# Optimization experiments

Hardware: AMD Instinct MI355X
Metric: run time of the kernel (lower is better)

## Reference

```python
import jax, jax.numpy as jnp
import numpy as np

B, T, D, H = 2, 1024, 1024, 16
K = D            # key_dim = hidden * expand_k (1.0)
V = 2 * D        # value_dim = hidden * expand_v (2.0)
DK, DV = K // H, V // H
I = 2816         # SwiGLU intermediate
CONV = 4
EPS = 1e-6


def rmsnorm(x, w, eps=EPS):
    return x * jax.lax.rsqrt(jnp.mean(x * x, -1, keepdims=True) + eps) * w


def l2norm(x, eps=EPS):
    return x * jax.lax.rsqrt(jnp.sum(x * x, -1, keepdims=True) + eps)


def short_conv(x, w):
    # depthwise causal conv1d (kernel CONV, no bias) + silu; x [B,T,C], w [C,CONV]
    kern = w.T[:, None, :]  # [CONV, 1, C]
    y = jax.lax.conv_general_dilated(
        x, kern, (1,), [(CONV - 1, 0)],
        dimension_numbers=('NWC', 'WIO', 'NWC'),
        feature_group_count=x.shape[-1])
    return jax.nn.silu(y)


def setup_inputs() -> dict:
    key = jax.random.key(0)
    ks = jax.random.split(key, 20)
    p = lambda i, shape, s=0.02: jax.random.normal(ks[i], shape, jnp.float32) * s
    return dict(
        x=jax.random.normal(ks[0], (B, T, D), jnp.float32),
        norm1_w=jnp.ones((D,), jnp.float32),
        wq=p(1, (D, K)), wk=p(2, (D, K)), wv=p(3, (D, V)),
        conv_q=p(4, (K, CONV), 0.3), conv_k=p(5, (K, CONV), 0.3), conv_v=p(6, (V, CONV), 0.3),
        wb=p(7, (D, H)), wa=p(8, (D, H)),
        A_log=jnp.log(jax.random.uniform(ks[9], (H,), jnp.float32, 1.0, 16.0)),
        dt_bias=jnp.log(jnp.expm1(jax.random.uniform(ks[10], (H,), jnp.float32, 0.001, 0.1))),
        wg=p(11, (D, V)),
        o_norm_w=jnp.ones((DV,), jnp.float32),
        wo=p(12, (V, D)),
        norm2_w=jnp.ones((D,), jnp.float32),
        w1=p(13, (D, I)), w2=p(14, (I, D)), w3=p(15, (D, I)),
    )


def reference(x, norm1_w, wq, wk, wv, conv_q, conv_k, conv_v, wb, wa,
              A_log, dt_bias, wg, o_norm_w, wo, norm2_w, w1, w2, w3):
    h = rmsnorm(x, norm1_w)
    # projections + short causal conv (silu)
    q = short_conv(h @ wq, conv_q).reshape(B, T, H, DK)
    k = short_conv(h @ wk, conv_k).reshape(B, T, H, DK)
    v = short_conv(h @ wv, conv_v).reshape(B, T, H, DV)
    q = l2norm(q) * (DK ** -0.5)
    k = l2norm(k)
    beta = jax.nn.sigmoid(h @ wb)                              # [B,T,H]
    # mamba-style decay gate: g = -exp(A_log) * softplus(a + dt_bias)
    g = -jnp.exp(A_log) * jax.nn.softplus(h @ wa + dt_bias)   # [B,T,H]

    # gated delta rule: S_t = exp(g_t)*S_{t-1}; u_t = beta_t*(v_t - k_t^T S_t);
    # S_t += k_t u_t^T; o_t = q_t^T S_t
    def step(S, inp):
        qt, kt, vt, gt, bt = inp                               # [B,H,*]
        S = S * jnp.exp(gt)[..., None, None]
        u = (vt - jnp.einsum('bhk,bhkv->bhv', kt, S)) * bt[..., None]
        S = S + kt[..., None] * u[:, :, None, :]
        ot = jnp.einsum('bhk,bhkv->bhv', qt, S)
        return S, ot

    S0 = jnp.zeros((B, H, DK, DV), x.dtype)
    seq = (q.transpose(1, 0, 2, 3), k.transpose(1, 0, 2, 3),
           v.transpose(1, 0, 2, 3), g.transpose(1, 0, 2), beta.transpose(1, 0, 2))
    _, o = jax.lax.scan(step, S0, seq)
    o = o.transpose(1, 0, 2, 3)                                # [B,T,H,DV]

    # output gate: per-head RMSNorm * swish(gate), then out-projection
    gate = (h @ wg).reshape(B, T, H, DV)
    o = rmsnorm(o, o_norm_w) * gate * jax.nn.sigmoid(gate)
    x = x + o.reshape(B, T, V) @ wo

    # SwiGLU MLP with residual
    h2 = rmsnorm(x, norm2_w)
    return x + (jax.nn.silu(h2 @ w1) * (h2 @ w3)) @ w2
```

## Files before the change

kernel.cpp:

```cpp
#include <hip/hip_runtime.h>
#include <stdint.h>

typedef unsigned short u16;
typedef float f32x4 __attribute__((ext_vector_type(4)));
typedef __bf16 bf16x8 __attribute__((ext_vector_type(8)));
typedef unsigned short u16x8 __attribute__((ext_vector_type(8)));

#define N1P 6400

__device__ __forceinline__ u16 f2bf(float f) {
    union { float f; uint32_t u; } v; v.f = f;
    uint32_t u = v.u;
    return (u16)((u + 0x7FFFu + ((u >> 16) & 1u)) >> 16);
}
__device__ __forceinline__ float bf2f(u16 h) {
    union { uint32_t u; float f; } v; v.u = ((uint32_t)h) << 16; return v.f;
}
__device__ __forceinline__ float sigm(float x) { return 1.f / (1.f + __expf(-x)); }

__device__ __forceinline__ void async16(const u16* g, u16* l) {
    __builtin_amdgcn_global_load_lds((const __attribute__((address_space(1))) void*)g,
                                     (__attribute__((address_space(3))) void*)l, 16, 0, 0);
}

__device__ __forceinline__ int swz64(int row, int col) {
    return row * 128 + ((((col >> 3) ^ (row & 7)) << 3) + (col & 7)) * 2;
}
__device__ __forceinline__ bf16x8 frag64(const u16* m, int rowbase, int lane, int kk) {
    const int row = rowbase + (lane & 15);
    const int unit = (lane >> 4) + (kk << 2);
    return *(const bf16x8*)((const char*)m + row * 128 + ((unit ^ (row & 7)) << 4));
}

struct TJob { const float* src; u16* dst; int rows, cols, rowOff, rowStride, nOut, blkBase, gx, mode; };
struct TJobs { TJob j[10]; };

__global__ __launch_bounds__(256) void k_transpose_all(TJobs jobs, int njobs) {
    __shared__ float tile[32][33];
    const int bid = blockIdx.x;
    int ji = 0;
#pragma unroll
    for (int i = 1; i < 10; ++i)
        if (i < njobs && bid >= jobs.j[i].blkBase) ji = i;
    const TJob J = jobs.j[ji];
    const int bx = bid - J.blkBase;
    const int n0 = (bx % J.gx) * 32, k0 = (bx / J.gx) * 32;
    const int tx = threadIdx.x, ty = threadIdx.y;
#pragma unroll
    for (int j = 0; j < 32; j += 8) {
        int r = k0 + ty + j, c = n0 + tx;
        tile[ty + j][tx] = (r < J.rows && c < J.cols) ? J.src[(size_t)r * J.cols + c] : 0.f;
    }
    __syncthreads();
#pragma unroll
    for (int j = 0; j < 32; j += 8) {
        int n = n0 + ty + j, k = k0 + tx;
        if (n < J.nOut) {
            int drow = (J.mode == 0) ? (J.rowOff + n * J.rowStride)
                                     : (J.rowOff + ((n >> 4) << 5) + (n & 15));
            J.dst[(size_t)drow * J.rows + k] = f2bf(tile[tx][ty + j]);
        }
    }
}

__global__ __launch_bounds__(256) void k_rmsnorm(const float* __restrict__ x, const float* __restrict__ w,
                                                 u16* __restrict__ out) {
    const int row = blockIdx.x, tid = threadIdx.x, lane = tid & 63, wave = tid >> 6;
    const float4 v = ((const float4*)(x + (size_t)row * 1024))[tid];
    float ss = v.x * v.x + v.y * v.y + v.z * v.z + v.w * v.w;
#pragma unroll
    for (int o = 1; o < 64; o <<= 1) ss += __shfl_xor(ss, o);
    __shared__ float sred[4];
    if (lane == 0) sred[wave] = ss;
    __syncthreads();
    const float tot = sred[0] + sred[1] + sred[2] + sred[3];
    const float rn = rsqrtf(tot * (1.f / 1024.f) + 1e-6f);
    const float4 wv = ((const float4*)w)[tid];
    uint2 pk;
    pk.x = (uint32_t)f2bf(v.x * rn * wv.x) | ((uint32_t)f2bf(v.y * rn * wv.y) << 16);
    pk.y = (uint32_t)f2bf(v.z * rn * wv.z) | ((uint32_t)f2bf(v.w * rn * wv.w) << 16);
    *(uint2*)&out[(size_t)row * 1024 + tid * 4] = pk;
}

template <int EPI>
__global__ __launch_bounds__(512, 2) void k_gemm256(const u16* __restrict__ A, const u16* __restrict__ Bt,
                                                    u16* __restrict__ Cout, int N, int Kd) {
    __shared__ __align__(16) u16 L[65536];
    const int q8 = (int)gridDim.x >> 3;
    const int bid = blockIdx.x;
    const int wg = (bid & 7) * q8 + (bid >> 3);
    const int bm = wg & 7, bn = wg >> 3;
    const int tid = threadIdx.x, lane = tid & 63, wave = tid >> 6;
    const int wm = wave >> 2, wn = wave & 3;

    const int scol = ((tid & 7) ^ ((tid >> 3) & 7)) * 8;
    const u16* gA = A + (size_t)(bm * 256 + (tid >> 3)) * Kd + scol;
    const u16* gB = Bt + (size_t)(bn * 256 + (tid >> 3)) * Kd + scol;
    u16* dstT = L + tid * 8;

    const int NT = Kd >> 6;
    const int NI = NT >> 1;

    auto issue = [&](const u16* g, int mtx, int kt, int h) {
        u16* d = dstT + (kt & 1) * 32768 + mtx * 16384 + h * 8192;
        const u16* s = g + (size_t)(h * 128) * Kd + kt * 64;
        async16(s, d);
        async16(s + (size_t)64 * Kd, d + 4096);
    };

    issue(gB, 1, 0, 0); issue(gB, 1, 0, 1);
    issue(gA, 0, 0, 0); issue(gA, 0, 0, 1);
    issue(gB, 1, 1, 0); issue(gB, 1, 1, 1);
    asm volatile("s_waitcnt vmcnt(4)" ::: "memory");
    __builtin_amdgcn_s_barrier();

    f32x4 acc[8][4] = {};
    bf16x8 bq[4][2];

    for (int i = 0; i < NI; ++i) {
        const int kt0 = 2 * i;
#pragma unroll
        for (int p = 0; p < 8; ++p) {
            const int half = p >> 2;
            const int q = p & 3;
            const u16* Ab = L + half * 32768;
            const u16* Bb = L + half * 32768 + 16384;
            if (q == 0) {
#pragma unroll
                for (int ni = 0; ni < 4; ++ni)
#pragma unroll
                    for (int kk = 0; kk < 2; ++kk)
                        bq[ni][kk] = frag64(Bb, wn * 64 + ni * 16, lane, kk);
            }
            bf16x8 af[2][2];
#pragma unroll
            for (int j = 0; j < 2; ++j)
#pragma unroll
                for (int kk = 0; kk < 2; ++kk)
                    af[j][kk] = frag64(Ab, wm * 128 + (2 * q + j) * 16, lane, kk);
            if (p == 0) { if (kt0 + 1 < NT) issue(gA, 0, kt0 + 1, 0); }
            if (p == 1) { if (kt0 + 1 < NT) issue(gA, 0, kt0 + 1, 1);
                          if (kt0 + 2 < NT) issue(gB, 1, kt0 + 2, 0); }
            if (p == 2) { if (kt0 + 2 < NT) issue(gB, 1, kt0 + 2, 1); }
            if (p == 4) { if (kt0 + 2 < NT) issue(gA, 0, kt0 + 2, 0); }
            if (p == 5) { if (kt0 + 2 < NT) issue(gA, 0, kt0 + 2, 1);
                          if (kt0 + 3 < NT) issue(gB, 1, kt0 + 3, 0); }
            if (p == 6) { if (kt0 + 3 < NT) issue(gB, 1, kt0 + 3, 1); }
            if (p == 3) { if (i + 1 < NI) { asm volatile("s_waitcnt vmcnt(4)" ::: "memory"); }
                          else            { asm volatile("s_waitcnt vmcnt(0)" ::: "memory"); } }
            if (p == 7) { if (i + 1 < NI) { asm volatile("s_waitcnt vmcnt(4)" ::: "memory"); } }
            __builtin_amdgcn_s_barrier();
            __builtin_amdgcn_s_setprio(1);
#pragma unroll
            for (int j = 0; j < 2; ++j)
#pragma unroll
                for (int ni = 0; ni < 4; ++ni)
#pragma unroll
                    for (int kk = 0; kk < 2; ++kk)
                        acc[2 * q + j][ni] = __builtin_amdgcn_mfma_f32_16x16x32_bf16(
                            af[j][kk], bq[ni][kk], acc[2 * q + j][ni], 0, 0, 0);
            __builtin_amdgcn_s_setprio(0);
            __builtin_amdgcn_s_barrier();
        }
    }

    const int rsub = (lane >> 4) * 4, csub = lane & 15;
    if constexpr (EPI == 2) {
        u16* ct = L;
#pragma unroll
        for (int r = 0; r < 2; ++r) {
            if (wm == r) {
#pragma unroll
                for (int mi = 0; mi < 8; ++mi)
#pragma unroll
                    for (int ni = 0; ni < 4; ++ni)
#pragma unroll
                        for (int rr = 0; rr < 4; ++rr)
                            ct[(mi * 16 + rsub + rr) * 264 + wn * 64 + ni * 16 + csub] =
                                f2bf(acc[mi][ni][rr]);
            }
            __syncthreads();
#pragma unroll
            for (int k = 0; k < 8; ++k) {
                const int f = (tid + k * 512) * 8;
                const int r2 = f >> 8, c = f & 255;
                *(u16x8*)&Cout[(size_t)(bm * 256 + r * 128 + r2) * N + bn * 256 + c] =
                    *(const u16x8*)&ct[r2 * 264 + c];
            }
            __syncthreads();
        }
    } else {
        u16* ct = L;
#pragma unroll
        for (int mi = 0; mi < 8; ++mi)
#pragma unroll
            for (int g = 0; g < 2; ++g)
#pragma unroll
                for (int rr = 0; rr < 4; ++rr) {
                    const float u1 = acc[mi][2 * g][rr];
                    const float u3 = acc[mi][2 * g + 1][rr];
                    ct[(wm * 128 + mi * 16 + rsub + rr) * 132 + wn * 32 + g * 16 + csub] =
                        f2bf(u1 * sigm(u1) * u3);
                }
        __syncthreads();
#pragma unroll
        for (int k = 0; k < 8; ++k) {
            const int f = (tid + k * 512) * 8;
            const int r2 = f >> 7, c = f & 127;
            *(u16x8*)&Cout[(size_t)(bm * 256 + r2) * N + bn * 128 + c] =
                *(const u16x8*)&ct[r2 * 132 + c];
        }
    }
}

__global__ __launch_bounds__(512) void k_gemm_skinny(const u16* __restrict__ A, const u16* __restrict__ Bt,
                                                     float* __restrict__ Cout, const float* __restrict__ Res,
                                                     int N, int Kd) {
    __shared__ __align__(16) char smem[49152];
    u16* Asb = (u16*)smem;
    u16* Bsb = (u16*)(smem + 32768);
    const int q = (int)gridDim.x >> 3;
    const int bid = blockIdx.x;
    const int wg = (bid & 7) * q + (bid >> 3);
    const int bm = wg & 15, bn = wg >> 4;
    const int tid = threadIdx.x, lane = tid & 63, wave = tid >> 6;
    const int wm = wave >> 1, wn = wave & 1;

    const int srow = tid >> 3;
    const int scol = ((tid & 7) ^ ((tid >> 3) & 7)) * 8;
    const u16* gA = A + (size_t)(bm * 128 + srow) * Kd + scol;
    const u16* gB = Bt + (size_t)(bn * 64 + srow) * Kd + scol;

    f32x4 acc[2][2] = {};
    const int NT = Kd >> 6;

    async16(gA, Asb + wave * 512);
    async16(gA + (size_t)64 * Kd, Asb + 4096 + wave * 512);
    async16(gB, Bsb + wave * 512);
    asm volatile("s_waitcnt vmcnt(0)" ::: "memory");
    __syncthreads();

    int buf = 0;
    for (int t = 0; t < NT; ++t) {
        if (t + 1 < NT) {
            const int k0 = (t + 1) << 6;
            const int ba = (buf ^ 1) * 8192, bb2 = (buf ^ 1) * 4096;
            async16(gA + k0, Asb + ba + wave * 512);
            async16(gA + (size_t)64 * Kd + k0, Asb + ba + 4096 + wave * 512);
            async16(gB + k0, Bsb + bb2 + wave * 512);
        }
        const u16* Ab = Asb + buf * 8192;
        const u16* Bb = Bsb + buf * 4096;
#pragma unroll
        for (int kk = 0; kk < 2; ++kk) {
            bf16x8 af[2], bfr[2];
#pragma unroll
            for (int mi = 0; mi < 2; ++mi) af[mi] = frag64(Ab, wm * 32 + mi * 16, lane, kk);
#pragma unroll
            for (int ni = 0; ni < 2; ++ni) bfr[ni] = frag64(Bb, wn * 32 + ni * 16, lane, kk);
#pragma unroll
            for (int mi = 0; mi < 2; ++mi)
#pragma unroll
                for (int ni = 0; ni < 2; ++ni)
                    acc[mi][ni] = __builtin_amdgcn_mfma_f32_16x16x32_bf16(af[mi], bfr[ni], acc[mi][ni], 0, 0, 0);
        }
        asm volatile("s_waitcnt vmcnt(0)" ::: "memory");
        __syncthreads();
        buf ^= 1;
    }

    const int rsub = (lane >> 4) * 4;
    const int csub = lane & 15;
    float* ctile = (float*)smem;
#pragma unroll
    for (int mi = 0; mi < 2; ++mi)
#pragma unroll
        for (int ni = 0; ni < 2; ++ni)
#pragma unroll
            for (int r = 0; r < 4; ++r)
                ctile[(wm * 32 + mi * 16 + rsub + r) * 68 + wn * 32 + ni * 16 + csub] = acc[mi][ni][r];
    __syncthreads();
#pragma unroll
    for (int k = 0; k < 4; ++k) {
        const int f = (tid + k * 512) * 4;
        const int r = f >> 6, c = f & 63;
        float4 v = *(const float4*)&ctile[r * 68 + c];
        const float4 rv = *(const float4*)&Res[(size_t)(bm * 128 + r) * N + bn * 64 + c];
        v.x += rv.x; v.y += rv.y; v.z += rv.z; v.w += rv.w;
        *(float4*)&Cout[(size_t)(bm * 128 + r) * N + bn * 64 + c] = v;
    }
}

__global__ __launch_bounds__(256) void k_conv(const u16* __restrict__ P, const float* __restrict__ cwq,
                                              const float* __restrict__ cwk, const float* __restrict__ cwv,
                                              const float* __restrict__ A_log, const float* __restrict__ dtb,
                                              u16* __restrict__ Qb, u16* __restrict__ Kb,
                                              u16* __restrict__ Vb, float* __restrict__ Gl,
                                              float* __restrict__ Bbuf) {
    const int bid = blockIdx.x;
    const int row = (bid & 7) * 256 + (bid >> 3);
    const int t = row & 1023;
    const int tid = threadIdx.x;
    const long prow = (long)row * N1P;
#pragma unroll
    for (int p = 0; p < 2; ++p) {
        const int g = p * 256 + tid;
        const int c = g * 8;
        u16x8 taps[4];
#pragma unroll
        for (int j = 0; j < 4; ++j) {
            const int tt = t - 3 + j;
            if (tt >= 0) taps[j] = *(const u16x8*)&P[prow + (long)(j - 3) * N1P + c];
            else         taps[j] = u16x8{};
        }
        const float* cw = (c < 1024) ? (cwq + c * 4)
                          : (c < 2048) ? (cwk + (c - 1024) * 4)
                                       : (cwv + (c - 2048) * 4);
        float y[8];
#pragma unroll
        for (int e = 0; e < 8; ++e) {
            const float4 w = ((const float4*)cw)[e];
            float v = bf2f(taps[0][e]) * w.x + bf2f(taps[1][e]) * w.y +
                      bf2f(taps[2][e]) * w.z + bf2f(taps[3][e]) * w.w;
            y[e] = v * sigm(v);
        }
        if (c < 2048) {
            float ss = 0.f;
#pragma unroll
            for (int e = 0; e < 8; ++e) ss += y[e] * y[e];
            ss += __shfl_xor(ss, 1); ss += __shfl_xor(ss, 2); ss += __shfl_xor(ss, 4);
            const float rn = rsqrtf(ss + 1e-6f);
            const float sc = (c < 1024) ? rn * 0.125f : rn;
            u16x8 o;
#pragma unroll
            for (int e = 0; e < 8; ++e) o[e] = f2bf(y[e] * sc);
            if (c < 1024) *(u16x8*)&Qb[(size_t)row * 1024 + c] = o;
            else          *(u16x8*)&Kb[(size_t)row * 1024 + (c - 1024)] = o;
        } else {
            u16x8 o;
#pragma unroll
            for (int e = 0; e < 8; ++e) o[e] = f2bf(y[e]);
            *(u16x8*)&Vb[(size_t)row * 2048 + (c - 2048)] = o;
        }
    }
    if (tid < 32) {
        const int h = tid & 15;
        const float val = bf2f(P[prow + 4096 + tid]);
        if (tid < 16) {
            Bbuf[(size_t)row * 16 + h] = sigm(val);
        } else {
            const float a = val + dtb[h];
            const float sp = (a > 15.f) ? a : log1pf(__expf(a));
            Gl[(size_t)row * 16 + h] = -__expf(A_log[h]) * sp;
        }
    }
}

__global__ __launch_bounds__(256) void k_scan1(
    const u16* __restrict__ Qb, const u16* __restrict__ Kb, const u16* __restrict__ Vb,
    const float* __restrict__ Gl, const float* __restrict__ Bb,
    u16* __restrict__ CHW, u16* __restrict__ CHM, u16* __restrict__ CHQc,
    u16* __restrict__ CHKcT, u16* __restrict__ CHU0T, float* __restrict__ CHcC) {
    __shared__ __align__(16) char sm[66048];
    u16* Ql   = (u16*)(sm);
    u16* Kl   = (u16*)(sm + 8192);
    u16* VTb  = (u16*)(sm + 16384);
    u16* KT1b = (u16*)(sm + 32768);
    u16* Mim  = (u16*)(sm + 40960);
    u16* MTim = (u16*)(sm + 49152);
    u16* Tb   = (u16*)(sm + 57344);
    float* Tl    = (float*)sm;
    float* gcs   = (float*)(sm + 65536);
    float* betal = (float*)(sm + 65792);

    const int blk = blockIdx.x;
    const int bb = blk >> 8, h = (blk >> 4) & 15, ch = blk & 15;
    const int bhc = blk;
    const int tid = threadIdx.x, lane = tid & 63, wave = tid >> 6;
    const long rowbase = (long)bb * 1024 + ch * 64;

    if (tid < 64) {
        gcs[tid] = Gl[(rowbase + tid) * 16 + h];
        betal[tid] = Bb[(rowbase + tid) * 16 + h];
    }
    for (int u = tid; u < 512; u += 256) {
        int r = u >> 3, c8 = u & 7;
        uint4 kv = *(const uint4*)&Kb[(rowbase + r) * 1024 + h * 64 + c8 * 8];
        uint4 qv = *(const uint4*)&Qb[(rowbase + r) * 1024 + h * 64 + c8 * 8];
        int b = r * 128 + ((c8 ^ (r & 7)) << 4);
        *(uint4*)((char*)Kl + b) = kv;
        *(uint4*)((char*)Ql + b) = qv;
    }
    __syncthreads();
    if (wave == 0) {
        float g = gcs[lane];
#pragma unroll
        for (int off = 1; off < 64; off <<= 1) {
            float n = __shfl_up(g, off, 64);
            if (lane >= off) g += n;
        }
        gcs[lane] = g;
    }
    for (int u = tid; u < 1024; u += 256) {
        int r = u >> 4, c8 = u & 15;
        u16x8 vv = *(const u16x8*)&Vb[(rowbase + r) * 2048 + h * 128 + c8 * 8];
        float bsc = betal[r];
#pragma unroll
        for (int j = 0; j < 8; ++j) {
            int dv = c8 * 8 + j;
            *(u16*)((char*)VTb + swz64(dv, r)) = f2bf(bf2f(vv[j]) * bsc);
        }
    }
    f32x4 aQK[4] = {}, aKK[4] = {};
#pragma unroll
    for (int nt = 0; nt < 4; ++nt)
#pragma unroll
        for (int kk = 0; kk < 2; ++kk) {
            bf16x8 bq = frag64(Kl, nt * 16, lane, kk);
            aQK[nt] = __builtin_amdgcn_mfma_f32_16x16x32_bf16(frag64(Ql, wave * 16, lane, kk), bq, aQK[nt], 0, 0, 0);
            aKK[nt] = __builtin_amdgcn_mfma_f32_16x16x32_bf16(frag64(Kl, wave * 16, lane, kk), bq, aKK[nt], 0, 0, 0);
        }
    __syncthreads();

    const float gcsC = gcs[63];
    float am[4][4];
#pragma unroll
    for (int nt = 0; nt < 4; ++nt)
#pragma unroll
        for (int reg = 0; reg < 4; ++reg) {
            int t = wave * 16 + ((lane >> 4) << 2) + reg;
            int i = nt * 16 + (lane & 15);
            float dec = __expf(gcs[t] - gcs[i]);
            float mv = (i <= t) ? dec * aQK[nt][reg] : 0.f;
            *(u16*)((char*)CHM + (size_t)bhc * 8192 + swz64(t, i)) = f2bf(mv);
            float a = (i < t) ? betal[t] * dec * aKK[nt][reg] : 0.f;
            am[nt][reg] = -a;
            u16 amb = f2bf(-a);
            *(u16*)((char*)Mim + swz64(t, i)) = amb;
            *(u16*)((char*)MTim + swz64(i, t)) = amb;
        }
    for (int e = tid; e < 4096; e += 256) {
        int r = e >> 6, c = e & 63;
        int ib = swz64(r, c);
        float qv = bf2f(*(const u16*)((const char*)Ql + ib)) * __expf(gcs[r]);
        *(u16*)((char*)CHQc + (size_t)bhc * 8192 + ib) = f2bf(qv);
        float kv = bf2f(*(const u16*)((const char*)Kl + ib));
        int ob = swz64(c, r);
        *(u16*)((char*)KT1b + ob) = f2bf(kv * betal[r] * __expf(gcs[r]));
        *(u16*)((char*)CHKcT + (size_t)bhc * 8192 + ob) = f2bf(kv * __expf(gcsC - gcs[r]));
    }
    if (tid == 0) CHcC[bhc] = __expf(gcsC);
    __syncthreads();

#pragma unroll
    for (int nt = 0; nt < 4; ++nt)
#pragma unroll
        for (int reg = 0; reg < 4; ++reg) {
            int t = wave * 16 + ((lane >> 4) << 2) + reg;
            int i = nt * 16 + (lane & 15);
            float tv = (t == i) ? 1.f : am[nt][reg];
            Tl[t * 64 + i] = tv;
            *(u16*)((char*)Tb + swz64(t, i)) = f2bf(tv);
        }
    __syncthreads();

    const int hi = wave * 16 + 15;
#pragma unroll
    for (int j = 1; j <= 5; ++j) {
        f32x4 aM[4] = {};
#pragma unroll
        for (int nt = 0; nt < 4; ++nt) {
            if (nt * 16 > hi - (1 << j)) continue;
#pragma unroll
            for (int kk = 0; kk < 2; ++kk) {
                if (kk * 32 > hi) break;
                aM[nt] = __builtin_amdgcn_mfma_f32_16x16x32_bf16(
                    frag64(Mim, wave * 16, lane, kk), frag64(MTim, nt * 16, lane, kk), aM[nt], 0, 0, 0);
            }
        }
        __syncthreads();
#pragma unroll
        for (int nt = 0; nt < 4; ++nt)
#pragma unroll
            for (int reg = 0; reg < 4; ++reg) {
                int t = wave * 16 + ((lane >> 4) << 2) + reg;
                int i = nt * 16 + (lane & 15);
                float mv = (t - i >= (1 << j)) ? aM[nt][reg] : 0.f;
                u16 mb = f2bf(mv);
                *(u16*)((char*)Mim + swz64(t, i)) = mb;
                *(u16*)((char*)MTim + swz64(i, t)) = mb;
            }
        __syncthreads();
        f32x4 aT[4];
#pragma unroll
        for (int nt = 0; nt < 4; ++nt)
#pragma unroll
            for (int reg = 0; reg < 4; ++reg) {
                int t = wave * 16 + ((lane >> 4) << 2) + reg;
                int i = nt * 16 + (lane & 15);
                aT[nt][reg] = Tl[t * 64 + i];
            }
#pragma unroll
        for (int nt = 0; nt < 4; ++nt) {
            if (nt * 16 > hi - (1 << j)) continue;
#pragma unroll
            for (int kk = 0; kk < 2; ++kk) {
                if (kk * 32 > hi) break;
                aT[nt] = __builtin_amdgcn_mfma_f32_16x16x32_bf16(
                    frag64(Tb, wave * 16, lane, kk), frag64(MTim, nt * 16, lane, kk), aT[nt], 0, 0, 0);
            }
        }
#pragma unroll
        for (int nt = 0; nt < 4; ++nt)
#pragma unroll
            for (int reg = 0; reg < 4; ++reg) {
                int t = wave * 16 + ((lane >> 4) << 2) + reg;
                int i = nt * 16 + (lane & 15);
                Tl[t * 64 + i] = aT[nt][reg];
                *(u16*)((char*)Tb + swz64(t, i)) = f2bf(aT[nt][reg]);
            }
    }
    __syncthreads();

    {
        f32x4 aW[4] = {};
#pragma unroll
        for (int nt = 0; nt < 4; ++nt)
#pragma unroll
            for (int kk = 0; kk < 2; ++kk) {
                if (kk * 32 > hi) break;
                aW[nt] = __builtin_amdgcn_mfma_f32_16x16x32_bf16(
                    frag64(Tb, wave * 16, lane, kk), frag64(KT1b, nt * 16, lane, kk), aW[nt], 0, 0, 0);
            }
#pragma unroll
        for (int nt = 0; nt < 4; ++nt)
#pragma unroll
            for (int reg = 0; reg < 4; ++reg) {
                int r = wave * 16 + ((lane >> 4) << 2) + reg;
                int c = nt * 16 + (lane & 15);
                *(u16*)((char*)CHW + (size_t)bhc * 8192 + swz64(r, c)) = f2bf(aW[nt][reg]);
            }
    }
#pragma unroll
    for (int rt = 0; rt < 2; ++rt) {
        f32x4 aU[4] = {};
        int rb = (wave * 2 + rt) * 16;
#pragma unroll
        for (int nt = 0; nt < 4; ++nt)
#pragma unroll
            for (int kk = 0; kk < 2; ++kk) {
                if (kk * 32 > nt * 16 + 15) continue;
                aU[nt] = __builtin_amdgcn_mfma_f32_16x16x32_bf16(
                    frag64(VTb, rb, lane, kk), frag64(Tb, nt * 16, lane, kk), aU[nt], 0, 0, 0);
            }
#pragma unroll
        for (int nt = 0; nt < 4; ++nt)
#pragma unroll
            for (int reg = 0; reg < 4; ++reg) {
                int dv = rb + ((lane >> 4) << 2) + reg;
                int c = nt * 16 + (lane & 15);
                *(u16*)((char*)CHU0T + (size_t)bhc * 16384 + swz64(dv, c)) = f2bf(aU[nt][reg]);
            }
    }
}

__global__ __launch_bounds__(256) void k_scan2(
    const u16* __restrict__ CHW, const u16* __restrict__ CHKcT, const u16* __restrict__ CHU0T,
    const float* __restrict__ CHcC, u16* __restrict__ CHu, u16* __restrict__ CHS0) {
    __shared__ __align__(16) u16 stg[2][3 * 4096];
    __shared__ __align__(16) u16 STb[4096], uTl[4096];
    __shared__ float ST[64 * 66];
    const int blk = blockIdx.x;
    const int bb = blk >> 5, h = (blk >> 1) & 15, dvh = blk & 1;
    const int bh = bb * 16 + h;
    const int tid = threadIdx.x, lane = tid & 63, wave = tid >> 6;

    for (int e = tid; e < 64 * 66; e += 256) ST[e] = 0.f;
    for (int e = tid; e < 4096; e += 256) STb[e] = 0;

    auto stage = [&](int buf, int ch) {
        const size_t base = (size_t)(bh * 16 + ch);
        const u16* srcs[3] = { CHW + base * 4096, CHKcT + base * 4096,
                               CHU0T + base * 8192 + dvh * 4096 };
#pragma unroll
        for (int s = 0; s < 3; ++s)
#pragma unroll
            for (int r = 0; r < 2; ++r) {
                int ub = r * 256 + wave * 64;
                async16(srcs[s] + (size_t)(ub + lane) * 8, &stg[buf][s * 4096 + ub * 8]);
            }
    };
    stage(0, 0);
    for (int ch = 0; ch < 16; ++ch) {
        const int cur = ch & 1;
        asm volatile("s_waitcnt vmcnt(0)" ::: "memory");
        __syncthreads();
        if (ch < 15) stage(cur ^ 1, ch + 1);
        const u16* sW = &stg[cur][0];
        const u16* sKcT = &stg[cur][4096];
        const u16* sU0 = &stg[cur][8192];
        {
            f32x4 acc[4] = {};
#pragma unroll
            for (int nt = 0; nt < 4; ++nt)
#pragma unroll
                for (int kk = 0; kk < 2; ++kk)
                    acc[nt] = __builtin_amdgcn_mfma_f32_16x16x32_bf16(
                        frag64(STb, wave * 16, lane, kk), frag64(sW, nt * 16, lane, kk), acc[nt], 0, 0, 0);
            const size_t ubase = ((size_t)(bh * 16 + ch) * 2 + dvh) * 8192;
#pragma unroll
            for (int nt = 0; nt < 4; ++nt)
#pragma unroll
                for (int reg = 0; reg < 4; ++reg) {
                    int dv = wave * 16 + ((lane >> 4) << 2) + reg;
                    int c = nt * 16 + (lane & 15);
                    int b = swz64(dv, c);
                    float u0 = bf2f(*(const u16*)((const char*)sU0 + b));
                    u16 uv = f2bf(u0 - acc[nt][reg]);
                    *(u16*)((char*)uTl + b) = uv;
                    *(u16*)((char*)CHu + ubase + b) = uv;
                }
        }
        __syncthreads();
        f32x4 accS[4] = {};
#pragma unroll
        for (int nt = 0; nt < 4; ++nt)
#pragma unroll
            for (int kk = 0; kk < 2; ++kk)
                accS[nt] = __builtin_amdgcn_mfma_f32_16x16x32_bf16(
                    frag64(uTl, wave * 16, lane, kk), frag64(sKcT, nt * 16, lane, kk), accS[nt], 0, 0, 0);
        __syncthreads();
        const float cC = CHcC[bh * 16 + ch];
        const size_t sbase = ((size_t)(bh * 16 + ch + 1) * 2 + dvh) * 8192;
#pragma unroll
        for (int nt = 0; nt < 4; ++nt)
#pragma unroll
            for (int reg = 0; reg < 4; ++reg) {
                int rr = wave * 16 + ((lane >> 4) << 2) + reg;
                int cc = nt * 16 + (lane & 15);
                float ns = cC * ST[rr * 66 + cc] + accS[nt][reg];
                ST[rr * 66 + cc] = ns;
                u16 nb = f2bf(ns);
                *(u16*)((char*)STb + swz64(rr, cc)) = nb;
                if (ch < 15) *(u16*)((char*)CHS0 + sbase + swz64(rr, cc)) = nb;
            }
    }
}

__global__ __launch_bounds__(256) void k_scan3(
    const u16* __restrict__ CHM, const u16* __restrict__ CHQc, const u16* __restrict__ CHu,
    const u16* __restrict__ CHS0, const u16* __restrict__ P, const float* __restrict__ onw,
    u16* __restrict__ OG) {
    __shared__ __align__(16) char sm3[65536];
    u16* sM  = (u16*)sm3;
    u16* sQc = (u16*)(sm3 + 8192);
    u16* sU  = (u16*)(sm3 + 16384);
    u16* sS0 = (u16*)(sm3 + 32768);
    u16* sPg = (u16*)(sm3 + 49152);
    const int blk = blockIdx.x;
    const int bb = blk >> 8, h = (blk >> 4) & 15, ch = blk & 15;
    const size_t bhc = blk;
    const int tid = threadIdx.x, lane = tid & 63, wave = tid >> 6;
    const bool hasS0 = (ch != 0);

#pragma unroll
    for (int r = 0; r < 2; ++r) {
        const int ub = r * 256 + wave * 64;
        async16(CHM + bhc * 4096 + (size_t)(ub + lane) * 8, sM + ub * 8);
        async16(CHQc + bhc * 4096 + (size_t)(ub + lane) * 8, sQc + ub * 8);
#pragma unroll
        for (int d = 0; d < 2; ++d) {
            async16(CHu + (bhc * 2 + d) * 4096 + (size_t)(ub + lane) * 8, sU + d * 4096 + ub * 8);
            if (hasS0)
                async16(CHS0 + (bhc * 2 + d) * 4096 + (size_t)(ub + lane) * 8, sS0 + d * 4096 + ub * 8);
        }
    }
    const long prow0 = ((long)bb * 1024 + ch * 64) * N1P + 4128 + h * 128;
#pragma unroll
    for (int k = 0; k < 4; ++k) {
        const int i = tid + k * 256;
        const int row = i >> 4, seg = i & 15;
        async16(P + prow0 + (long)row * N1P + seg * 8, sPg + i * 8);
    }
    asm volatile("s_waitcnt vmcnt(0)" ::: "memory");
    __syncthreads();

    f32x4 accO[2][4] = {};
#pragma unroll
    for (int d = 0; d < 2; ++d)
#pragma unroll
        for (int nt = 0; nt < 4; ++nt)
#pragma unroll
            for (int kk = 0; kk < 2; ++kk) {
                accO[d][nt] = __builtin_amdgcn_mfma_f32_16x16x32_bf16(
                    frag64(sM, wave * 16, lane, kk), frag64(sU + d * 4096, nt * 16, lane, kk),
                    accO[d][nt], 0, 0, 0);
                if (hasS0)
                    accO[d][nt] = __builtin_amdgcn_mfma_f32_16x16x32_bf16(
                        frag64(sQc, wave * 16, lane, kk), frag64(sS0 + d * 4096, nt * 16, lane, kk),
                        accO[d][nt], 0, 0, 0);
            }

    const int rsub = (lane >> 4) * 4, csub = lane & 15;
    float rn[4];
#pragma unroll
    for (int reg = 0; reg < 4; ++reg) {
        float ss = 0.f;
#pragma unroll
        for (int d = 0; d < 2; ++d)
#pragma unroll
            for (int nt = 0; nt < 4; ++nt) {
                const float v = accO[d][nt][reg];
                ss += v * v;
            }
        ss += __shfl_xor(ss, 1); ss += __shfl_xor(ss, 2);
        ss += __shfl_xor(ss, 4); ss += __shfl_xor(ss, 8);
        rn[reg] = rsqrtf(ss * (1.f / 128.f) + 1e-6f);
    }
    __syncthreads();
    u16* ct = (u16*)sm3;
#pragma unroll
    for (int d = 0; d < 2; ++d)
#pragma unroll
        for (int nt = 0; nt < 4; ++nt)
#pragma unroll
            for (int reg = 0; reg < 4; ++reg) {
                const int rr = wave * 16 + rsub + reg;
                const int dv = d * 64 + nt * 16 + csub;
                const float g = bf2f(sPg[rr * 128 + dv]);
                const float val = accO[d][nt][reg] * rn[reg] * onw[dv] * g * sigm(g);
                ct[rr * 136 + dv] = f2bf(val);
            }
    __syncthreads();
#pragma unroll
    for (int k = 0; k < 4; ++k) {
        const int f = (tid + k * 256) * 8;
        const int r2 = f >> 7, c = f & 127;
        *(u16x8*)&OG[(size_t)(bb * 1024 + ch * 64 + r2) * 2048 + h * 128 + c] =
            *(const u16x8*)&ct[r2 * 136 + c];
    }
}

extern "C" void kernel_launch(void* const* d_in, const int* in_sizes, int n_in,
                              void* d_out, int out_size, void* d_ws, size_t ws_size,
                              hipStream_t stream) {
    const float* x   = (const float*)d_in[0];
    const float* n1w = (const float*)d_in[1];
    const float* wq  = (const float*)d_in[2];
    const float* wk  = (const float*)d_in[3];
    const float* wv  = (const float*)d_in[4];
    const float* cq  = (const float*)d_in[5];
    const float* ck  = (const float*)d_in[6];
    const float* cv  = (const float*)d_in[7];
    const float* wb  = (const float*)d_in[8];
    const float* wa  = (const float*)d_in[9];
    const float* Alg = (const float*)d_in[10];
    const float* dtb = (const float*)d_in[11];
    const float* wg  = (const float*)d_in[12];
    const float* onw = (const float*)d_in[13];
    const float* wo  = (const float*)d_in[14];
    const float* n2w = (const float*)d_in[15];
    const float* w1  = (const float*)d_in[16];
    const float* w2  = (const float*)d_in[17];
    const float* w3  = (const float*)d_in[18];

    if (ws_size < 128190464ULL) return;

    char* ws = (char*)d_ws;
    u16*   WcatT = (u16*)(ws + 0);
    u16*   WoT   = (u16*)(ws + 13107200);
    u16*   W13T  = (u16*)(ws + 17301504);
    u16*   W2T   = (u16*)(ws + 28835840);
    u16*   hA    = (u16*)(ws + 34603008);
    u16*   P     = (u16*)(ws + 38797312);
    u16*   Qb    = (u16*)(ws + 65011712);
    u16*   Kb    = (u16*)(ws + 69206016);
    u16*   Vb    = (u16*)(ws + 73400320);
    float* Gl    = (float*)(ws + 81788928);
    float* Bbf   = (float*)(ws + 81920000);
    float* X2    = (float*)(ws + 82051072);
    u16*   CHKcT = (u16*)(ws + 98828288);
    u16*   CHU0T = (u16*)(ws + 103022592);
    float* CHcC  = (float*)(ws + 111411200);
    u16*   CHu   = (u16*)(ws + 111413248);
    u16*   CHS0  = (u16*)(ws + 119801856);
    u16*   CHW   = WcatT;
    u16*   CHM   = (u16*)(ws + 4194304);
    u16*   CHQc  = (u16*)(ws + 8388608);
    u16*   Mm  = Qb;
    u16*   OG  = Vb;
    u16*   h2A = hA;

    TJobs tj;
    tj.j[0] = { wq, WcatT, 1024, 1024,    0, 1, 1024,     0, 32, 0 };
    tj.j[1] = { wk, WcatT, 1024, 1024, 1024, 1, 1024,  1024, 32, 0 };
    tj.j[2] = { wv, WcatT, 1024, 2048, 2048, 1, 2048,  2048, 64, 0 };
    tj.j[3] = { wb, WcatT, 1024,   16, 4096, 1,   16,  4096,  1, 0 };
    tj.j[4] = { wa, WcatT, 1024,   16, 4112, 1,   16,  4128,  1, 0 };
    tj.j[5] = { wg, WcatT, 1024, 2048, 4128, 1, 2272,  4160, 71, 0 };
    tj.j[6] = { wo, WoT,   2048, 1024,    0, 1, 1024,  6432, 32, 0 };
    tj.j[7] = { w1, W13T,  1024, 2816,    0, 1, 2816,  8480, 88, 1 };
    tj.j[8] = { w3, W13T,  1024, 2816,   16, 1, 2816, 11296, 88, 1 };
    tj.j[9] = { w2, W2T,   2816, 1024,    0, 1, 1024, 14112, 32, 0 };
    k_transpose_all<<<16928, dim3(32, 8), 0, stream>>>(tj, 10);

    k_rmsnorm<<<2048, 256, 0, stream>>>(x, n1w, hA);
    k_gemm256<2><<<200, 512, 0, stream>>>(hA, WcatT, P, N1P, 1024);

    k_conv<<<2048, 256, 0, stream>>>(P, cq, ck, cv, Alg, dtb, Qb, Kb, Vb, Gl, Bbf);

    k_scan1<<<512, 256, 0, stream>>>(Qb, Kb, Vb, Gl, Bbf, CHW, CHM, CHQc, CHKcT, CHU0T, CHcC);
    k_scan2<<<64, 256, 0, stream>>>(CHW, CHKcT, CHU0T, CHcC, CHu, CHS0);
    k_scan3<<<512, 256, 0, stream>>>(CHM, CHQc, CHu, CHS0, P, onw, OG);

    k_gemm_skinny<<<256, 512, 0, stream>>>(OG, WoT, X2, x, 1024, 2048);

    k_rmsnorm<<<2048, 256, 0, stream>>>(X2, n2w, h2A);
    k_gemm256<3><<<176, 512, 0, stream>>>(h2A, W13T, Mm, 2816, 1024);
    k_gemm_skinny<<<256, 512, 0, stream>>>(Mm, W2T, (float*)d_out, X2, 1024, 2816);
}
```

Measured before the change: 259.0 us.

## Precompute chunk transition matrices in scan1 to shorten sequential scan2 chain

Rewrites the inter-chunk state recurrence algebraically. scan1 now precomputes per chunk A = -W^T KcT and B = U0^T KcT, so scan2 performs a single matmul per chunk (S·A + B, plus the decayed old state) instead of two dependent matmuls with an intermediate u write. The u correction (U0 - S0·W) moves into the parallel scan3 kernel. This takes work off the serial 64-block scan2 in exchange for extra MFMA work and global writes in scan1 and scan3, and it adds one more bf16 rounding of the transition matrix A.

```diff
diff --git a/kernel.cpp b/kernel.cpp
--- a/kernel.cpp
+++ b/kernel.cpp
@@ -360,7 +360,8 @@
     const u16* __restrict__ Qb, const u16* __restrict__ Kb, const u16* __restrict__ Vb,
     const float* __restrict__ Gl, const float* __restrict__ Bb,
     u16* __restrict__ CHW, u16* __restrict__ CHM, u16* __restrict__ CHQc,
-    u16* __restrict__ CHKcT, u16* __restrict__ CHU0T, float* __restrict__ CHcC) {
+    u16* __restrict__ CHKcT, u16* __restrict__ CHU0T, float* __restrict__ CHcC,
+    u16* __restrict__ CHA2m, u16* __restrict__ CHB) {
     __shared__ __align__(16) char sm[66048];
     u16* Ql   = (u16*)(sm);
     u16* Kl   = (u16*)(sm + 8192);
@@ -522,6 +523,15 @@
     }
     __syncthreads();
 
+    u16* KcTl = Ql;
+    u16* WTl  = Kl;
+    u16* U0Tl = Mim;
+#pragma unroll
+    for (int r = 0; r < 2; ++r) {
+        const int g = r * 256 + tid;
+        async16(CHKcT + (size_t)bhc * 4096 + (size_t)g * 8, KcTl + g * 8);
+    }
+
     {
         f32x4 aW[4] = {};
 #pragma unroll
@@ -538,7 +548,9 @@
             for (int reg = 0; reg < 4; ++reg) {
                 int r = wave * 16 + ((lane >> 4) << 2) + reg;
                 int c = nt * 16 + (lane & 15);
-                *(u16*)((char*)CHW + (size_t)bhc * 8192 + swz64(r, c)) = f2bf(aW[nt][reg]);
+                u16 wv = f2bf(aW[nt][reg]);
+                *(u16*)((char*)CHW + (size_t)bhc * 8192 + swz64(r, c)) = wv;
+                *(u16*)((char*)WTl + swz64(c, r)) = wv;
             }
     }
 #pragma unroll
@@ -559,16 +571,57 @@
             for (int reg = 0; reg < 4; ++reg) {
                 int dv = rb + ((lane >> 4) << 2) + reg;
                 int c = nt * 16 + (lane & 15);
-                *(u16*)((char*)CHU0T + (size_t)bhc * 16384 + swz64(dv, c)) = f2bf(aU[nt][reg]);
+                u16 uv = f2bf(aU[nt][reg]);
+                *(u16*)((char*)CHU0T + (size_t)bhc * 16384 + swz64(dv, c)) = uv;
+                *(u16*)((char*)U0Tl + swz64(dv, c)) = uv;
+            }
+    }
+    asm volatile("s_waitcnt vmcnt(0)" ::: "memory");
+    __syncthreads();
+
+    {
+        f32x4 aA[4] = {};
+#pragma unroll
+        for (int nt = 0; nt < 4; ++nt)
+#pragma unroll
+            for (int kk = 0; kk < 2; ++kk)
+                aA[nt] = __builtin_amdgcn_mfma_f32_16x16x32_bf16(
+                    frag64(WTl, wave * 16, lane, kk), frag64(KcTl, nt * 16, lane, kk), aA[nt], 0, 0, 0);
+#pragma unroll
+        for (int nt = 0; nt < 4; ++nt)
+#pragma unroll
+            for (int reg = 0; reg < 4; ++reg) {
+                int kI = wave * 16 + ((lane >> 4) << 2) + reg;
+                int dk = nt * 16 + (lane & 15);
+                *(u16*)((char*)CHA2m + (size_t)bhc * 8192 + swz64(dk, kI)) = f2bf(-aA[nt][reg]);
+            }
+    }
+#pragma unroll
+    for (int rt = 0; rt < 2; ++rt) {
+        f32x4 aB[4] = {};
+        int rb = (wave * 2 + rt) * 16;
+#pragma unroll
+        for (int nt = 0; nt < 4; ++nt)
+#pragma unroll
+            for (int kk = 0; kk < 2; ++kk)
+                aB[nt] = __builtin_amdgcn_mfma_f32_16x16x32_bf16(
+                    frag64(U0Tl, rb, lane, kk), frag64(KcTl, nt * 16, lane, kk), aB[nt], 0, 0, 0);
+#pragma unroll
+        for (int nt = 0; nt < 4; ++nt)
+#pragma unroll
+            for (int reg = 0; reg < 4; ++reg) {
+                int dv = rb + ((lane >> 4) << 2) + reg;
+                int dk = nt * 16 + (lane & 15);
+                *(u16*)((char*)CHB + (size_t)bhc * 16384 + swz64(dv, dk)) = f2bf(aB[nt][reg]);
             }
     }
 }
 
 __global__ __launch_bounds__(256) void k_scan2(
-    const u16* __restrict__ CHW, const u16* __restrict__ CHKcT, const u16* __restrict__ CHU0T,
-    const float* __restrict__ CHcC, u16* __restrict__ CHu, u16* __restrict__ CHS0) {
-    __shared__ __align__(16) u16 stg[2][3 * 4096];
-    __shared__ __align__(16) u16 STb[4096], uTl[4096];
+    const u16* __restrict__ CHA2m, const u16* __restrict__ CHB,
+    const float* __restrict__ CHcC, u16* __restrict__ CHS0) {
+    __shared__ __align__(16) u16 stg[2][8192];
+    __shared__ __align__(16) u16 STb[4096];
     __shared__ float ST[64 * 66];
     const int blk = blockIdx.x;
     const int bb = blk >> 5, h = (blk >> 1) & 15, dvh = blk & 1;
@@ -580,83 +633,60 @@
 
     auto stage = [&](int buf, int ch) {
         const size_t base = (size_t)(bh * 16 + ch);
-        const u16* srcs[3] = { CHW + base * 4096, CHKcT + base * 4096,
-                               CHU0T + base * 8192 + dvh * 4096 };
-#pragma unroll
-        for (int s = 0; s < 3; ++s)
-#pragma unroll
-            for (int r = 0; r < 2; ++r) {
-                int ub = r * 256 + wave * 64;
-                async16(srcs[s] + (size_t)(ub + lane) * 8, &stg[buf][s * 4096 + ub * 8]);
-            }
+        const u16* sA = CHA2m + base * 4096;
+        const u16* sB = CHB + base * 8192 + dvh * 4096;
+#pragma unroll
+        for (int r = 0; r < 2; ++r) {
+            const int g = r * 256 + tid;
+            async16(sA + (size_t)g * 8, &stg[buf][g * 8]);
+            async16(sB + (size_t)g * 8, &stg[buf][4096 + g * 8]);
+        }
     };
     stage(0, 0);
+    int cur = 0;
     for (int ch = 0; ch < 16; ++ch) {
-        const int cur = ch & 1;
         asm volatile("s_waitcnt vmcnt(0)" ::: "memory");
         __syncthreads();
         if (ch < 15) stage(cur ^ 1, ch + 1);
-        const u16* sW = &stg[cur][0];
-        const u16* sKcT = &stg[cur][4096];
-        const u16* sU0 = &stg[cur][8192];
-        {
-            f32x4 acc[4] = {};
-#pragma unroll
-            for (int nt = 0; nt < 4; ++nt)
-#pragma unroll
-                for (int kk = 0; kk < 2; ++kk)
-                    acc[nt] = __builtin_amdgcn_mfma_f32_16x16x32_bf16(
-                        frag64(STb, wave * 16, lane, kk), frag64(sW, nt * 16, lane, kk), acc[nt], 0, 0, 0);
-            const size_t ubase = ((size_t)(bh * 16 + ch) * 2 + dvh) * 8192;
-#pragma unroll
-            for (int nt = 0; nt < 4; ++nt)
-#pragma unroll
-                for (int reg = 0; reg < 4; ++reg) {
-                    int dv = wave * 16 + ((lane >> 4) << 2) + reg;
-                    int c = nt * 16 + (lane & 15);
-                    int b = swz64(dv, c);
-                    float u0 = bf2f(*(const u16*)((const char*)sU0 + b));
-                    u16 uv = f2bf(u0 - acc[nt][reg]);
-                    *(u16*)((char*)uTl + b) = uv;
-                    *(u16*)((char*)CHu + ubase + b) = uv;
-                }
-        }
-        __syncthreads();
-        f32x4 accS[4] = {};
+        const u16* sA2 = &stg[cur][0];
+        const u16* sB = &stg[cur][4096];
+        f32x4 acc[4] = {};
 #pragma unroll
         for (int nt = 0; nt < 4; ++nt)
 #pragma unroll
             for (int kk = 0; kk < 2; ++kk)
-                accS[nt] = __builtin_amdgcn_mfma_f32_16x16x32_bf16(
-                    frag64(uTl, wave * 16, lane, kk), frag64(sKcT, nt * 16, lane, kk), accS[nt], 0, 0, 0);
-        __syncthreads();
+                acc[nt] = __builtin_amdgcn_mfma_f32_16x16x32_bf16(
+                    frag64(STb, wave * 16, lane, kk), frag64(sA2, nt * 16, lane, kk), acc[nt], 0, 0, 0);
         const float cC = CHcC[bh * 16 + ch];
         const size_t sbase = ((size_t)(bh * 16 + ch + 1) * 2 + dvh) * 8192;
 #pragma unroll
         for (int nt = 0; nt < 4; ++nt)
 #pragma unroll
             for (int reg = 0; reg < 4; ++reg) {
-                int rr = wave * 16 + ((lane >> 4) << 2) + reg;
-                int cc = nt * 16 + (lane & 15);
-                float ns = cC * ST[rr * 66 + cc] + accS[nt][reg];
+                const int rr = wave * 16 + ((lane >> 4) << 2) + reg;
+                const int cc = nt * 16 + (lane & 15);
+                const float bv = bf2f(*(const u16*)((const char*)sB + swz64(rr, cc)));
+                const float ns = cC * ST[rr * 66 + cc] + acc[nt][reg] + bv;
                 ST[rr * 66 + cc] = ns;
-                u16 nb = f2bf(ns);
+                const u16 nb = f2bf(ns);
                 *(u16*)((char*)STb + swz64(rr, cc)) = nb;
                 if (ch < 15) *(u16*)((char*)CHS0 + sbase + swz64(rr, cc)) = nb;
             }
+        cur ^= 1;
     }
 }
 
 __global__ __launch_bounds__(256) void k_scan3(
-    const u16* __restrict__ CHM, const u16* __restrict__ CHQc, const u16* __restrict__ CHu,
-    const u16* __restrict__ CHS0, const u16* __restrict__ P, const float* __restrict__ onw,
-    u16* __restrict__ OG) {
-    __shared__ __align__(16) char sm3[65536];
+    const u16* __restrict__ CHM, const u16* __restrict__ CHQc, const u16* __restrict__ CHW,
+    const u16* __restrict__ CHU0T, const u16* __restrict__ CHS0, const u16* __restrict__ P,
+    const float* __restrict__ onw, u16* __restrict__ OG) {
+    __shared__ __align__(16) char sm3[73728];
     u16* sM  = (u16*)sm3;
     u16* sQc = (u16*)(sm3 + 8192);
-    u16* sU  = (u16*)(sm3 + 16384);
-    u16* sS0 = (u16*)(sm3 + 32768);
-    u16* sPg = (u16*)(sm3 + 49152);
+    u16* sW  = (u16*)(sm3 + 16384);
+    u16* sU  = (u16*)(sm3 + 24576);
+    u16* sS0 = (u16*)(sm3 + 40960);
+    u16* sPg = (u16*)(sm3 + 57344);
     const int blk = blockIdx.x;
     const int bb = blk >> 8, h = (blk >> 4) & 15, ch = blk & 15;
     const size_t bhc = blk;
@@ -665,14 +695,15 @@
 
 #pragma unroll
     for (int r = 0; r < 2; ++r) {
-        const int ub = r * 256 + wave * 64;
-        async16(CHM + bhc * 4096 + (size_t)(ub + lane) * 8, sM + ub * 8);
-        async16(CHQc + bhc * 4096 + (size_t)(ub + lane) * 8, sQc + ub * 8);
+        const int g = r * 256 + tid;
+        async16(CHM + bhc * 4096 + (size_t)g * 8, sM + g * 8);
+        async16(CHQc + bhc * 4096 + (size_t)g * 8, sQc + g * 8);
+        async16(CHW + bhc * 4096 + (size_t)g * 8, sW + g * 8);
 #pragma unroll
         for (int d = 0; d < 2; ++d) {
-            async16(CHu + (bhc * 2 + d) * 4096 + (size_t)(ub + lane) * 8, sU + d * 4096 + ub * 8);
+            async16(CHU0T + (bhc * 2 + d) * 4096 + (size_t)g * 8, sU + d * 4096 + g * 8);
             if (hasS0)
-                async16(CHS0 + (bhc * 2 + d) * 4096 + (size_t)(ub + lane) * 8, sS0 + d * 4096 + ub * 8);
+                async16(CHS0 + (bhc * 2 + d) * 4096 + (size_t)g * 8, sS0 + d * 4096 + g * 8);
         }
     }
     const long prow0 = ((long)bb * 1024 + ch * 64) * N1P + 4128 + h * 128;
@@ -684,6 +715,30 @@
     }
     asm volatile("s_waitcnt vmcnt(0)" ::: "memory");
     __syncthreads();
+
+    if (hasS0) {
+#pragma unroll
+        for (int d = 0; d < 2; ++d) {
+            f32x4 au[4] = {};
+#pragma unroll
+            for (int nt = 0; nt < 4; ++nt)
+#pragma unroll
+                for (int kk = 0; kk < 2; ++kk)
+                    au[nt] = __builtin_amdgcn_mfma_f32_16x16x32_bf16(
+                        frag64(sS0 + d * 4096, wave * 16, lane, kk), frag64(sW, nt * 16, lane, kk),
+                        au[nt], 0, 0, 0);
+#pragma unroll
+            for (int nt = 0; nt < 4; ++nt)
+#pragma unroll
+                for (int reg = 0; reg < 4; ++reg) {
+                    const int dv = wave * 16 + ((lane >> 4) << 2) + reg;
+                    const int c = nt * 16 + (lane & 15);
+                    u16* p = (u16*)((char*)sU + d * 8192 + swz64(dv, c));
+                    *p = f2bf(bf2f(*p) - au[nt][reg]);
+                }
+        }
+        __syncthreads();
+    }
 
     f32x4 accO[2][4] = {};
 #pragma unroll
@@ -764,7 +819,7 @@
     const float* w2  = (const float*)d_in[17];
     const float* w3  = (const float*)d_in[18];
 
-    if (ws_size < 128190464ULL) return;
+    if (ws_size < 132384768ULL) return;
 
     char* ws = (char*)d_ws;
     u16*   WcatT = (u16*)(ws + 0);
@@ -782,8 +837,9 @@
     u16*   CHKcT = (u16*)(ws + 98828288);
     u16*   CHU0T = (u16*)(ws + 103022592);
     float* CHcC  = (float*)(ws + 111411200);
-    u16*   CHu   = (u16*)(ws + 111413248);
-    u16*   CHS0  = (u16*)(ws + 119801856);
+    u16*   CHA2m = (u16*)(ws + 111413248);
+    u16*   CHB   = (u16*)(ws + 115607552);
+    u16*   CHS0  = (u16*)(ws + 123996160);
     u16*   CHW   = WcatT;
     u16*   CHM   = (u16*)(ws + 4194304);
     u16*   CHQc  = (u16*)(ws + 8388608);
@@ -809,9 +865,10 @@
 
     k_conv<<<2048, 256, 0, stream>>>(P, cq, ck, cv, Alg, dtb, Qb, Kb, Vb, Gl, Bbf);
 
-    k_scan1<<<512, 256, 0, stream>>>(Qb, Kb, Vb, Gl, Bbf, CHW, CHM, CHQc, CHKcT, CHU0T, CHcC);
-    k_scan2<<<64, 256, 0, stream>>>(CHW, CHKcT, CHU0T, CHcC, CHu, CHS0);
-    k_scan3<<<512, 256, 0, stream>>>(CHM, CHQc, CHu, CHS0, P, onw, OG);
+    k_scan1<<<512, 256, 0, stream>>>(Qb, Kb, Vb, Gl, Bbf, CHW, CHM, CHQc, CHKcT, CHU0T, CHcC,
+                                     CHA2m, CHB);
+    k_scan2<<<64, 256, 0, stream>>>(CHA2m, CHB, CHcC, CHS0);
+    k_scan3<<<512, 256, 0, stream>>>(CHM, CHQc, CHW, CHU0T, CHS0, P, onw, OG);
 
     k_gemm_skinny<<<256, 512, 0, stream>>>(OG, WoT, X2, x, 1024, 2048);
 
```

Measured after the change: 243.9 us. -5.8%, faster.
